# Performance work log

Hardware: AMD Instinct MI355X
Metric: run time of the kernel (lower is better)

Reference implementation:

```python
import jax, jax.numpy as jnp
import numpy as np

# Standard icosahedron face list (20 faces over 12 vertices).
ICO_FACES = np.array([
    [0, 11, 5], [0, 5, 1], [0, 1, 7], [0, 7, 10], [0, 10, 11],
    [1, 5, 9], [5, 11, 4], [11, 10, 2], [10, 7, 6], [7, 1, 8],
    [3, 9, 4], [3, 4, 2], [3, 2, 6], [3, 6, 8], [3, 8, 9],
    [4, 9, 5], [2, 4, 11], [6, 2, 10], [8, 6, 7], [9, 8, 1],
], dtype=np.int64)


def _ico_face_adjacency():
    # Faces are adjacent iff they share an edge == share exactly 2 vertices.
    adj = np.zeros((20, 20), dtype=np.float32)
    for i in range(20):
        for j in range(i + 1, 20):
            if len(set(ICO_FACES[i]) & set(ICO_FACES[j])) == 2:
                adj[i, j] = adj[j, i] = 1.0
    return jnp.asarray(adj)


def setup_inputs() -> dict:
    key = jax.random.key(0)
    ks = jax.random.split(key, 9)
    B, D = 65536, 512
    def w(k, fan_in, fan_out):
        return jax.random.normal(k, (fan_in, fan_out), jnp.float32) * (1.0 / np.sqrt(fan_in))
    return {
        "z": jax.random.normal(ks[0], (B, D), jnp.float32),
        "W1": w(ks[1], D, 512), "b1": jnp.zeros((512,), jnp.float32),
        "W2": w(ks[2], 512, 256), "b2": jnp.zeros((256,), jnp.float32),
        "W3": w(ks[3], 256, 128), "b3": jnp.zeros((128,), jnp.float32),
        "W4": w(ks[4], 128, 20), "b4": jnp.zeros((20,), jnp.float32),
        "precomputed_adj": _ico_face_adjacency(),  # [20,20], zero diagonal
    }


def reference(z, W1, b1, W2, b2, W3, b3, W4, b4, precomputed_adj):
    # Eval path: dropout = identity, recon_loss = 0.
    h = jax.nn.relu(z @ W1 + b1)
    h = jax.nn.relu(h @ W2 + b2)
    h = jax.nn.relu(h @ W3 + b3)
    face_probs = jax.nn.sigmoid(h @ W4 + b4)          # [B, 20]
    face_mask = (face_probs > 0.5).astype(z.dtype)    # [B, 20]
    # outer(mask, mask) * precomputed adjacency; diagonal of adj is already 0,
    # reproducing the i != j condition of the original triple loop.
    adj_matrix = face_mask[:, :, None] * face_mask[:, None, :] * precomputed_adj  # [B,20,20]
    recon_loss = jnp.asarray(0.0, jnp.float32)
    return (adj_matrix, face_mask, face_probs, recon_loss)
```

## Files before the change

kernel.cpp:

```cpp
#include <hip/hip_runtime.h>
#include <math.h>

#define NT   1024
#define BR   32
#define TAU  1e-3f
#define LIST_CAP 65536

typedef _Float16 half8 __attribute__((ext_vector_type(8)));
typedef float    f32x4 __attribute__((ext_vector_type(4)));

#define SWZ(r) (((r)&7)<<4)

#define PACK_ELS 425984
#define OFF_LIST 16
#define OFF_PH   (16 + LIST_CAP*4)
#define OFF_PL   (OFF_PH + PACK_ELS*2)
#define WS_PACK_NEED (OFF_PL + PACK_ELS*2)
#define WS_F32_NEED  (16 + LIST_CAP*4)

__device__ __forceinline__ int p1(int c){ return ((c&7)<<6)|(c>>3); }
__device__ __forceinline__ int p2(int c){ return ((c&3)<<6)|(c>>2); }
__device__ __forceinline__ int p3(int c){ return ((c&1)<<6)|(c>>1); }

__global__ void pack_w(const float* __restrict__ W1, const float* __restrict__ W2,
                       const float* __restrict__ W3,
                       _Float16* __restrict__ PH, _Float16* __restrict__ PL) {
    int i = blockIdx.x * 256 + threadIdx.x;
    if (i >= PACK_ELS) return;
    const float* W; int N, KS, loc;
    if (i < 262144)            { W = W1; N = 512; KS = 16; loc = i; }
    else if (i < 393216)       { W = W2; N = 256; KS = 16; loc = i - 262144; }
    else                       { W = W3; N = 128; KS = 8;  loc = i - 393216; }
    int j   = loc & 7;
    int l   = (loc >> 3) & 63;
    int rest = loc >> 9;
    int ks  = rest & (KS - 1);
    int nt  = rest >> (KS == 16 ? 4 : 3);
    int k = ks * 32 + (l >> 4) * 8 + j;
    int n = nt * 16 + (l & 15);
    float v = W[k * N + n];
    _Float16 hi = (_Float16)v;
    _Float16 lo = (_Float16)(v - (float)hi);
    PH[i] = hi; PL[i] = lo;
}

template<int K, int N, int NTW, int MREP, bool SPLIT_OUT>
__device__ __forceinline__ void mfma_layer(const char* __restrict__ actIn,
    const _Float16* __restrict__ PH, const _Float16* __restrict__ PL,
    const float* __restrict__ bias,
    char* __restrict__ actOut, float* __restrict__ h3out,
    int nt0, int m0, int l)
{
    constexpr int KS = K / 32;
    const int r  = l & 15;
    const int kg = l >> 4;
    f32x4 acc[MREP][NTW];
#pragma unroll
    for (int t = 0; t < NTW; ++t) {
        float bb = bias[(nt0 + t) * 16 + r];
#pragma unroll
        for (int m = 0; m < MREP; ++m) acc[m][t] = (f32x4){bb, bb, bb, bb};
    }
    constexpr int loIn = BR * K * 2;

#define AADDR(m, ks) ((((((m0 + (m)) * 16 + r) * K + kg * 8 + (ks) * 32) * 2) ^ SWZ((m0 + (m)) * 16 + r)))
#define BIDX(t, ks)  (((size_t)((nt0 + (t)) * KS + (ks)) * 64 + l) * 8)

    half8 ah0[MREP], al0[MREP];
    half8 bh0[NTW],  bl0[NTW];
    half8 bh1[NTW],  bl1[NTW];
#pragma unroll
    for (int m = 0; m < MREP; ++m) {
        int ao = AADDR(m, 0);
        ah0[m] = *(const half8*)(actIn + ao);
        al0[m] = *(const half8*)(actIn + ao + loIn);
    }
#pragma unroll
    for (int t = 0; t < NTW; ++t) {
        bh0[t] = *(const half8*)(PH + BIDX(t, 0));
        bl0[t] = *(const half8*)(PL + BIDX(t, 0));
        bh1[t] = *(const half8*)(PH + BIDX(t, 1));
        bl1[t] = *(const half8*)(PL + BIDX(t, 1));
    }

#pragma unroll
    for (int ks = 0; ks < KS; ++ks) {
        half8 bh2[NTW], bl2[NTW], ahn[MREP], aln[MREP];
        if (ks + 2 < KS) {
#pragma unroll
            for (int t = 0; t < NTW; ++t) {
                bh2[t] = *(const half8*)(PH + BIDX(t, ks + 2));
                bl2[t] = *(const half8*)(PL + BIDX(t, ks + 2));
            }
        }
        if (ks + 1 < KS) {
#pragma unroll
            for (int m = 0; m < MREP; ++m) {
                int ao = AADDR(m, ks + 1);
                ahn[m] = *(const half8*)(actIn + ao);
                aln[m] = *(const half8*)(actIn + ao + loIn);
            }
        }
#pragma unroll
        for (int t = 0; t < NTW; ++t)
#pragma unroll
            for (int m = 0; m < MREP; ++m) {
                acc[m][t] = __builtin_amdgcn_mfma_f32_16x16x32_f16(ah0[m], bh0[t], acc[m][t], 0, 0, 0);
                acc[m][t] = __builtin_amdgcn_mfma_f32_16x16x32_f16(ah0[m], bl0[t], acc[m][t], 0, 0, 0);
                acc[m][t] = __builtin_amdgcn_mfma_f32_16x16x32_f16(al0[m], bh0[t], acc[m][t], 0, 0, 0);
            }
#pragma unroll
        for (int t = 0; t < NTW; ++t) {
            bh0[t] = bh1[t]; bl0[t] = bl1[t];
            bh1[t] = bh2[t]; bl1[t] = bl2[t];
        }
#pragma unroll
        for (int m = 0; m < MREP; ++m) { ah0[m] = ahn[m]; al0[m] = aln[m]; }
    }
#undef AADDR
#undef BIDX

    constexpr int loOut = BR * N * 2;
#pragma unroll
    for (int t = 0; t < NTW; ++t) {
        int n = (nt0 + t) * 16 + r;
#pragma unroll
        for (int m = 0; m < MREP; ++m)
#pragma unroll
        for (int b = 0; b < 4; ++b) {
            int rowD = (m0 + m) * 16 + kg * 4 + b;
            float v = acc[m][t][b];
            v = v > 0.f ? v : 0.f;
            if constexpr (SPLIT_OUT) {
                _Float16 hi = (_Float16)v;
                _Float16 lo = (_Float16)(v - (float)hi);
                int lin = (rowD * N + n) * 2;
                int sw  = lin ^ SWZ(rowD);
                *(_Float16*)(actOut + sw)         = hi;
                *(_Float16*)(actOut + sw + loOut) = lo;
            } else {
                h3out[rowD * 132 + n] = v;
            }
        }
    }
}

__global__ __launch_bounds__(NT, 4)
void dec_mfma(const float* __restrict__ z,
              const float* __restrict__ b1, const float* __restrict__ b2,
              const float* __restrict__ b3,
              const float* __restrict__ W4, const float* __restrict__ b4,
              const float* __restrict__ adj,
              const _Float16* __restrict__ PH, const _Float16* __restrict__ PL,
              float* __restrict__ out, int B,
              int* __restrict__ cnt, int* __restrict__ list)
{
    __shared__ __align__(16) char ldsA[65536];
    __shared__ __align__(16) char ldsB[65536];
    __shared__ float logitsS[BR * 20];
    __shared__ float maskS[BR * 20];
    __shared__ float adjS[400];

    const int tid = threadIdx.x;
    const int w   = tid >> 6;
    const int l   = tid & 63;
    const int rowBase = blockIdx.x * BR;

    const int O_MASK  = B * 400;
    const int O_PROBS = O_MASK + B * 20;
    const int O_LOSS  = O_PROBS + B * 20;

    if (tid < 400) adjS[tid] = adj[tid];

    {
        int r   = tid >> 5;
        int c16 = (tid & 31) * 16;
        const float4* zp = (const float4*)(z + (size_t)(rowBase + r) * 512 + c16);
        float4 f0 = zp[0], f1 = zp[1], f2 = zp[2], f3 = zp[3];
        float fv[16] = {f0.x,f0.y,f0.z,f0.w, f1.x,f1.y,f1.z,f1.w,
                        f2.x,f2.y,f2.z,f2.w, f3.x,f3.y,f3.z,f3.w};
        half8 hi0, hi1, lo0, lo1;
#pragma unroll
        for (int j = 0; j < 8; ++j) {
            _Float16 h = (_Float16)fv[j];
            hi0[j] = h; lo0[j] = (_Float16)(fv[j] - (float)h);
        }
#pragma unroll
        for (int j = 0; j < 8; ++j) {
            _Float16 h = (_Float16)fv[8 + j];
            hi1[j] = h; lo1[j] = (_Float16)(fv[8 + j] - (float)h);
        }
        int lin = (r * 512 + c16) * 2;
        int swz = SWZ(r);
        *(half8*)(ldsA + ((lin     ) ^ swz))          = hi0;
        *(half8*)(ldsA + ((lin + 16) ^ swz))          = hi1;
        *(half8*)(ldsA + ((lin     ) ^ swz) + 32768)  = lo0;
        *(half8*)(ldsA + ((lin + 16) ^ swz) + 32768)  = lo1;
    }
    __syncthreads();

    mfma_layer<512, 512, 2, 2, true >(ldsA, PH,          PL,          b1, ldsB, nullptr, w * 2, 0, l);
    __syncthreads();
    mfma_layer<512, 256, 1, 2, true >(ldsB, PH + 262144, PL + 262144, b2, ldsA, nullptr, w, 0, l);
    __syncthreads();
    mfma_layer<256, 128, 1, 1, false>(ldsA, PH + 393216, PL + 393216, b3, nullptr, (float*)ldsB, w & 7, w >> 3, l);
    __syncthreads();

    const float* h3 = (const float*)ldsB;
    for (int o = tid; o < BR * 20; o += NT) {
        int r = o / 20, c = o - r * 20;
        float acc = b4[c];
        for (int k = 0; k < 128; ++k)
            acc += h3[r * 132 + k] * W4[k * 20 + c];
        logitsS[o] = acc;
    }
    __syncthreads();

    if (tid < BR) {
        float mn = 1e30f;
#pragma unroll
        for (int c = 0; c < 20; ++c)
            mn = fminf(mn, fabsf(logitsS[tid * 20 + c]));
        if (mn < TAU) {
            int idx = atomicAdd(cnt, 1);
            if (idx < LIST_CAP) list[idx] = rowBase + tid;
        }
    }

    for (int o = tid; o < BR * 20; o += NT) {
        double lg = (double)logitsS[o];
        double p  = 1.0 / (1.0 + exp(-lg));
        out[O_PROBS + rowBase * 20 + o] = (float)p;
        float m = lg > 0.0 ? 1.0f : 0.0f;
        out[O_MASK + rowBase * 20 + o] = m;
        maskS[o] = m;
    }
    __syncthreads();

    for (int o = tid; o < BR * 20; o += NT) {
        int r = o / 20, ii = o - r * 20;
        float mri = maskS[r * 20 + ii];
        float* orow = &out[(rowBase + r) * 400 + ii * 20];
#pragma unroll
        for (int b = 0; b < 5; ++b) {
            float4 v;
            v.x = mri * maskS[r * 20 + 4*b+0] * adjS[ii * 20 + 4*b+0];
            v.y = mri * maskS[r * 20 + 4*b+1] * adjS[ii * 20 + 4*b+1];
            v.z = mri * maskS[r * 20 + 4*b+2] * adjS[ii * 20 + 4*b+2];
            v.w = mri * maskS[r * 20 + 4*b+3] * adjS[ii * 20 + 4*b+3];
            *(float4*)&orow[4*b] = v;
        }
    }

    if (blockIdx.x == 0 && tid == 0) out[O_LOSS] = 0.0f;
}

template<typename T, bool FLAG>
__global__ __launch_bounds__(256, 2)
void dec_fused(const float* __restrict__ z,
               const float* __restrict__ W1, const float* __restrict__ b1,
               const float* __restrict__ W2, const float* __restrict__ b2,
               const float* __restrict__ W3, const float* __restrict__ b3,
               const float* __restrict__ W4, const float* __restrict__ b4,
               const float* __restrict__ adj,
               float* __restrict__ out, int B,
               int* __restrict__ cnt, int* __restrict__ list)
{
    constexpr int STR = (sizeof(T) == 4) ? 20 : 17;
    __shared__ T     hT[512 * STR];
    __shared__ T     logitsS[16 * 20];
    __shared__ float maskS[16 * 20];
    __shared__ float adjS[400];

    const int tid = threadIdx.x;
    const int rg  = tid >> 6;
    const int cg  = tid & 63;
    const int r0  = rg * 4;
    const int rowBase = blockIdx.x * 16;

    const int O_MASK  = B * 400;
    const int O_PROBS = O_MASK + B * 20;
    const int O_LOSS  = O_PROBS + B * 20;

    for (int i = tid; i < 400; i += 256) adjS[i] = adj[i];
    for (int i = tid; i < 512 * 16; i += 256) {
        int k = i & 511, r = i >> 9;
        hT[k * STR + r] = (T)z[(rowBase + r) * 512 + k];
    }
    __syncthreads();
    {
        T a[4][8];
#pragma unroll
        for (int ri = 0; ri < 4; ++ri)
#pragma unroll
            for (int ci = 0; ci < 8; ++ci) a[ri][ci] = (T)0;
#pragma unroll 2
        for (int k = 0; k < 512; ++k) {
            T zr[4];
#pragma unroll
            for (int ri = 0; ri < 4; ++ri) zr[ri] = hT[k * STR + r0 + ri];
            const float4* w1p = (const float4*)(W1 + k * 512 + cg * 8);
            float4 w0 = w1p[0], w1v = w1p[1];
            T wv[8] = {(T)w0.x,(T)w0.y,(T)w0.z,(T)w0.w,
                       (T)w1v.x,(T)w1v.y,(T)w1v.z,(T)w1v.w};
#pragma unroll
            for (int ci = 0; ci < 8; ++ci)
#pragma unroll
                for (int ri = 0; ri < 4; ++ri)
                    a[ri][ci] += zr[ri] * wv[ci];
        }
        __syncthreads();
#pragma unroll
        for (int ci = 0; ci < 8; ++ci) {
            int c = cg * 8 + ci;
            T bb = (T)b1[c]; int cp = p1(c);
#pragma unroll
            for (int ri = 0; ri < 4; ++ri) {
                T v = a[ri][ci] + bb;
                hT[cp * STR + r0 + ri] = v > (T)0 ? v : (T)0;
            }
        }
        __syncthreads();
    }
    {
        T a[4][4];
#pragma unroll
        for (int ri = 0; ri < 4; ++ri)
#pragma unroll
            for (int ci = 0; ci < 4; ++ci) a[ri][ci] = (T)0;
#pragma unroll 2
        for (int k = 0; k < 512; ++k) {
            int kp = p1(k);
            T zr[4];
#pragma unroll
            for (int ri = 0; ri < 4; ++ri) zr[ri] = hT[kp * STR + r0 + ri];
            float4 wq = *(const float4*)(W2 + k * 256 + cg * 4);
            T wv[4] = {(T)wq.x,(T)wq.y,(T)wq.z,(T)wq.w};
#pragma unroll
            for (int ci = 0; ci < 4; ++ci)
#pragma unroll
                for (int ri = 0; ri < 4; ++ri)
                    a[ri][ci] += zr[ri] * wv[ci];
        }
        __syncthreads();
#pragma unroll
        for (int ci = 0; ci < 4; ++ci) {
            int c = cg * 4 + ci;
            T bb = (T)b2[c]; int cp = p2(c);
#pragma unroll
            for (int ri = 0; ri < 4; ++ri) {
                T v = a[ri][ci] + bb;
                hT[cp * STR + r0 + ri] = v > (T)0 ? v : (T)0;
            }
        }
        __syncthreads();
    }
    {
        T a[4][2];
#pragma unroll
        for (int ri = 0; ri < 4; ++ri)
#pragma unroll
            for (int ci = 0; ci < 2; ++ci) a[ri][ci] = (T)0;
#pragma unroll 2
        for (int k = 0; k < 256; ++k) {
            int kp = p2(k);
            T zr[4];
#pragma unroll
            for (int ri = 0; ri < 4; ++ri) zr[ri] = hT[kp * STR + r0 + ri];
            float2 wq = *(const float2*)(W3 + k * 128 + cg * 2);
            T wv[2] = {(T)wq.x,(T)wq.y};
#pragma unroll
            for (int ci = 0; ci < 2; ++ci)
#pragma unroll
                for (int ri = 0; ri < 4; ++ri)
                    a[ri][ci] += zr[ri] * wv[ci];
        }
        __syncthreads();
#pragma unroll
        for (int ci = 0; ci < 2; ++ci) {
            int c = cg * 2 + ci;
            T bb = (T)b3[c]; int cp = p3(c);
#pragma unroll
            for (int ri = 0; ri < 4; ++ri) {
                T v = a[ri][ci] + bb;
                hT[cp * STR + r0 + ri] = v > (T)0 ? v : (T)0;
            }
        }
        __syncthreads();
    }
    for (int o = tid; o < 16 * 20; o += 256) {
        int r = o / 20, c = o - r * 20;
        T acc = (T)b4[c];
        for (int k = 0; k < 128; ++k)
            acc += hT[p3(k) * STR + r] * (T)W4[k * 20 + c];
        logitsS[o] = acc;
    }
    __syncthreads();
    if constexpr (FLAG) {
        if (tid < 16) {
            float mn = 1e30f;
#pragma unroll
            for (int c = 0; c < 20; ++c)
                mn = fminf(mn, fabsf((float)logitsS[tid * 20 + c]));
            if (mn < TAU) {
                int idx = atomicAdd(cnt, 1);
                if (idx < LIST_CAP) list[idx] = rowBase + tid;
            }
        }
    }
    for (int o = tid; o < 16 * 20; o += 256) {
        double lg = (double)logitsS[o];
        double p  = 1.0 / (1.0 + exp(-lg));
        out[O_PROBS + rowBase * 20 + o] = (float)p;
        float m = lg > 0.0 ? 1.0f : 0.0f;
        out[O_MASK + rowBase * 20 + o] = m;
        maskS[o] = m;
    }
    __syncthreads();
    for (int o = tid; o < 16 * 20; o += 256) {
        int r = o / 20, ii = o - r * 20;
        float mri = maskS[r * 20 + ii];
        float* orow = &out[(rowBase + r) * 400 + ii * 20];
#pragma unroll
        for (int b = 0; b < 5; ++b) {
            float4 v;
            v.x = mri * maskS[r * 20 + 4*b+0] * adjS[ii * 20 + 4*b+0];
            v.y = mri * maskS[r * 20 + 4*b+1] * adjS[ii * 20 + 4*b+1];
            v.z = mri * maskS[r * 20 + 4*b+2] * adjS[ii * 20 + 4*b+2];
            v.w = mri * maskS[r * 20 + 4*b+3] * adjS[ii * 20 + 4*b+3];
            *(float4*)&orow[4*b] = v;
        }
    }
    if (blockIdx.x == 0 && tid == 0) out[O_LOSS] = 0.0f;
}

__global__ __launch_bounds__(256, 4)
void repair_rows(const float* __restrict__ z,
                 const float* __restrict__ W1, const float* __restrict__ b1,
                 const float* __restrict__ W2, const float* __restrict__ b2,
                 const float* __restrict__ W3, const float* __restrict__ b3,
                 const float* __restrict__ W4, const float* __restrict__ b4,
                 const float* __restrict__ adj,
                 float* __restrict__ out, int B,
                 const int* __restrict__ cnt, const int* __restrict__ list)
{
    __shared__ double bufA[512];
    __shared__ double bufB[512];
    __shared__ double lgS[20];
    __shared__ float  mskS[20];

    const int tid = threadIdx.x;
    const int O_MASK  = B * 400;
    const int O_PROBS = O_MASK + B * 20;

    int n = *cnt;
    if (n > LIST_CAP) n = LIST_CAP;

    for (int i = blockIdx.x; i < n; i += gridDim.x) {
        int row = list[i];
        for (int k = tid; k < 512; k += 256)
            bufA[k] = (double)z[(size_t)row * 512 + k];
        __syncthreads();
        {
            int c0 = tid, c1 = tid + 256;
            double a0 = (double)b1[c0], a1 = (double)b1[c1];
            for (int k = 0; k < 512; ++k) {
                double h = bufA[k];
                a0 += h * (double)W1[k * 512 + c0];
                a1 += h * (double)W1[k * 512 + c1];
            }
            __syncthreads();
            bufB[c0] = a0 > 0.0 ? a0 : 0.0;
            bufB[c1] = a1 > 0.0 ? a1 : 0.0;
            __syncthreads();
        }
        {
            double a0 = (double)b2[tid < 256 ? tid : 0];
            if (tid < 256)
                for (int k = 0; k < 512; ++k)
                    a0 += bufB[k] * (double)W2[k * 256 + tid];
            __syncthreads();
            if (tid < 256) bufA[tid] = a0 > 0.0 ? a0 : 0.0;
            __syncthreads();
        }
        {
            double a0 = (double)b3[tid < 128 ? tid : 0];
            if (tid < 128)
                for (int k = 0; k < 256; ++k)
                    a0 += bufA[k] * (double)W3[k * 128 + tid];
            __syncthreads();
            if (tid < 128) bufB[tid] = a0 > 0.0 ? a0 : 0.0;
            __syncthreads();
        }
        if (tid < 20) {
            double a0 = (double)b4[tid];
            for (int k = 0; k < 128; ++k)
                a0 += bufB[k] * (double)W4[k * 20 + tid];
            lgS[tid] = a0;
        }
        __syncthreads();
        if (tid < 20) {
            double lg = lgS[tid];
            out[O_PROBS + (size_t)row * 20 + tid] = (float)(1.0 / (1.0 + exp(-lg)));
            float m = lg > 0.0 ? 1.0f : 0.0f;
            out[O_MASK + (size_t)row * 20 + tid] = m;
            mskS[tid] = m;
        }
        __syncthreads();
        for (int o = tid; o < 400; o += 256) {
            int ii = o / 20, jj = o - ii * 20;
            out[(size_t)row * 400 + o] = mskS[ii] * mskS[jj] * adj[o];
        }
        __syncthreads();
    }
}

extern "C" void kernel_launch(void* const* d_in, const int* in_sizes, int n_in,
                              void* d_out, int out_size, void* d_ws, size_t ws_size,
                              hipStream_t stream) {
    const float* z   = (const float*)d_in[0];
    const float* W1  = (const float*)d_in[1];
    const float* b1  = (const float*)d_in[2];
    const float* W2  = (const float*)d_in[3];
    const float* b2  = (const float*)d_in[4];
    const float* W3  = (const float*)d_in[5];
    const float* b3  = (const float*)d_in[6];
    const float* W4  = (const float*)d_in[7];
    const float* b4  = (const float*)d_in[8];
    const float* adj = (const float*)d_in[9];
    float* out = (float*)d_out;

    const int B = in_sizes[0] / 512;

    if (ws_size >= (size_t)WS_PACK_NEED) {
        int* cnt  = (int*)d_ws;
        int* list = (int*)((char*)d_ws + OFF_LIST);
        _Float16* PH = (_Float16*)((char*)d_ws + OFF_PH);
        _Float16* PL = (_Float16*)((char*)d_ws + OFF_PL);
        hipMemsetAsync(d_ws, 0, 16, stream);
        hipLaunchKernelGGL(pack_w, dim3((PACK_ELS + 255) / 256), dim3(256), 0, stream,
                           W1, W2, W3, PH, PL);
        hipLaunchKernelGGL(dec_mfma, dim3(B / BR), dim3(NT), 0, stream,
                           z, b1, b2, b3, W4, b4, adj, PH, PL, out, B, cnt, list);
        hipLaunchKernelGGL(repair_rows, dim3(1024), dim3(256), 0, stream,
                           z, W1, b1, W2, b2, W3, b3, W4, b4, adj, out, B, cnt, list);
    } else if (ws_size >= (size_t)WS_F32_NEED) {
        int* cnt  = (int*)d_ws;
        int* list = (int*)((char*)d_ws + OFF_LIST);
        hipMemsetAsync(d_ws, 0, 16, stream);
        hipLaunchKernelGGL((dec_fused<float, true>), dim3(B / 16), dim3(256), 0, stream,
                           z, W1, b1, W2, b2, W3, b3, W4, b4, adj, out, B, cnt, list);
        hipLaunchKernelGGL(repair_rows, dim3(1024), dim3(256), 0, stream,
                           z, W1, b1, W2, b2, W3, b3, W4, b4, adj, out, B, cnt, list);
    } else {
        hipLaunchKernelGGL((dec_fused<double, false>), dim3(B / 16), dim3(256), 0, stream,
                           z, W1, b1, W2, b2, W3, b3, W4, b4, adj, out, B,
                           (int*)nullptr, (int*)nullptr);
    }
}
```

Baseline: 455.6 us.

## Hand-schedule weight prefetch with inline asm loads and explicit vmcnt waits

Replaces the compiler-scheduled weight-fragment prefetch with inline-asm global_load_dwordx4 into a three-slot ring buffer. Explicit s_waitcnt vmcnt counts and sched_barriers keep two k-steps of weight loads in flight across the MFMA block. Activation LDS reads move to the current k-step instead of being prefetched one step ahead, and s_setprio raises wave priority around the MFMA burst. This aims to stop the compiler from serializing or conservatively waiting on loads, at the cost of fragile hand-tuned wait counts and more exposed LDS latency.

After: 446.8 us. No clear change (-1.9%).

```diff
diff --git a/kernel.cpp b/kernel.cpp
--- a/kernel.cpp
+++ b/kernel.cpp
@@ -8,6 +8,7 @@
 
 typedef _Float16 half8 __attribute__((ext_vector_type(8)));
 typedef float    f32x4 __attribute__((ext_vector_type(4)));
+typedef unsigned int u32x4 __attribute__((ext_vector_type(4)));
 
 #define SWZ(r) (((r)&7)<<4)
 
@@ -44,6 +45,19 @@
     PH[i] = hi; PL[i] = lo;
 }
 
+__device__ __forceinline__ u32x4 agl(const _Float16* p) {
+    u32x4 d;
+    asm volatile("global_load_dwordx4 %0, %1, off" : "=v"(d) : "v"(p));
+    return d;
+}
+template<int NWAIT> __device__ __forceinline__ void waitv() {
+    if constexpr (NWAIT == 0)      asm volatile("s_waitcnt vmcnt(0)");
+    else if constexpr (NWAIT == 2) asm volatile("s_waitcnt vmcnt(2)");
+    else if constexpr (NWAIT == 4) asm volatile("s_waitcnt vmcnt(4)");
+    else                           asm volatile("s_waitcnt vmcnt(8)");
+    __builtin_amdgcn_sched_barrier(0);
+}
+
 template<int K, int N, int NTW, int MREP, bool SPLIT_OUT>
 __device__ __forceinline__ void mfma_layer(const char* __restrict__ actIn,
     const _Float16* __restrict__ PH, const _Float16* __restrict__ PL,
@@ -51,7 +65,8 @@
     char* __restrict__ actOut, float* __restrict__ h3out,
     int nt0, int m0, int l)
 {
-    constexpr int KS = K / 32;
+    constexpr int KS    = K / 32;
+    constexpr int BATCH = 2 * NTW;
     const int r  = l & 15;
     const int kg = l >> 4;
     f32x4 acc[MREP][NTW];
@@ -61,64 +76,56 @@
 #pragma unroll
         for (int m = 0; m < MREP; ++m) acc[m][t] = (f32x4){bb, bb, bb, bb};
     }
+    __builtin_amdgcn_sched_barrier(0);
     constexpr int loIn = BR * K * 2;
 
 #define AADDR(m, ks) ((((((m0 + (m)) * 16 + r) * K + kg * 8 + (ks) * 32) * 2) ^ SWZ((m0 + (m)) * 16 + r)))
-#define BIDX(t, ks)  (((size_t)((nt0 + (t)) * KS + (ks)) * 64 + l) * 8)
-
-    half8 ah0[MREP], al0[MREP];
-    half8 bh0[NTW],  bl0[NTW];
-    half8 bh1[NTW],  bl1[NTW];
-#pragma unroll
-    for (int m = 0; m < MREP; ++m) {
-        int ao = AADDR(m, 0);
-        ah0[m] = *(const half8*)(actIn + ao);
-        al0[m] = *(const half8*)(actIn + ao + loIn);
-    }
-#pragma unroll
-    for (int t = 0; t < NTW; ++t) {
-        bh0[t] = *(const half8*)(PH + BIDX(t, 0));
-        bl0[t] = *(const half8*)(PL + BIDX(t, 0));
-        bh1[t] = *(const half8*)(PH + BIDX(t, 1));
-        bl1[t] = *(const half8*)(PL + BIDX(t, 1));
-    }
+#define BOFF(t, ks)  (((size_t)((nt0 + (t)) * KS + (ks)) * 64 + l) * 8)
+
+    u32x4 Bh[3][NTW], Bl[3][NTW];
+#pragma unroll
+    for (int t = 0; t < NTW; ++t) { Bh[0][t] = agl(PH + BOFF(t, 0)); Bl[0][t] = agl(PL + BOFF(t, 0)); }
+#pragma unroll
+    for (int t = 0; t < NTW; ++t) { Bh[1][t] = agl(PH + BOFF(t, 1)); Bl[1][t] = agl(PL + BOFF(t, 1)); }
 
 #pragma unroll
     for (int ks = 0; ks < KS; ++ks) {
-        half8 bh2[NTW], bl2[NTW], ahn[MREP], aln[MREP];
+        const int cur = ks % 3, nx = (ks + 2) % 3;
         if (ks + 2 < KS) {
 #pragma unroll
             for (int t = 0; t < NTW; ++t) {
-                bh2[t] = *(const half8*)(PH + BIDX(t, ks + 2));
-                bl2[t] = *(const half8*)(PL + BIDX(t, ks + 2));
-            }
-        }
-        if (ks + 1 < KS) {
+                Bh[nx][t] = agl(PH + BOFF(t, ks + 2));
+                Bl[nx][t] = agl(PL + BOFF(t, ks + 2));
+            }
+        }
+        half8 ah[MREP], al[MREP];
+#pragma unroll
+        for (int m = 0; m < MREP; ++m) {
+            int ao = AADDR(m, ks);
+            ah[m] = *(const half8*)(actIn + ao);
+            al[m] = *(const half8*)(actIn + ao + loIn);
+        }
+        const int rem = KS - 1 - ks;
+        if (rem >= 2)      waitv<2 * BATCH>();
+        else if (rem == 1) waitv<BATCH>();
+        else               waitv<0>();
+        __builtin_amdgcn_s_setprio(1);
+#pragma unroll
+        for (int t = 0; t < NTW; ++t) {
+            half8 bh = __builtin_bit_cast(half8, Bh[cur][t]);
+            half8 bl = __builtin_bit_cast(half8, Bl[cur][t]);
 #pragma unroll
             for (int m = 0; m < MREP; ++m) {
-                int ao = AADDR(m, ks + 1);
-                ahn[m] = *(const half8*)(actIn + ao);
-                aln[m] = *(const half8*)(actIn + ao + loIn);
-            }
-        }
-#pragma unroll
-        for (int t = 0; t < NTW; ++t)
-#pragma unroll
-            for (int m = 0; m < MREP; ++m) {
-                acc[m][t] = __builtin_amdgcn_mfma_f32_16x16x32_f16(ah0[m], bh0[t], acc[m][t], 0, 0, 0);
-                acc[m][t] = __builtin_amdgcn_mfma_f32_16x16x32_f16(ah0[m], bl0[t], acc[m][t], 0, 0, 0);
-                acc[m][t] = __builtin_amdgcn_mfma_f32_16x16x32_f16(al0[m], bh0[t], acc[m][t], 0, 0, 0);
-            }
-#pragma unroll
-        for (int t = 0; t < NTW; ++t) {
-            bh0[t] = bh1[t]; bl0[t] = bl1[t];
-            bh1[t] = bh2[t]; bl1[t] = bl2[t];
-        }
-#pragma unroll
-        for (int m = 0; m < MREP; ++m) { ah0[m] = ahn[m]; al0[m] = aln[m]; }
+                acc[m][t] = __builtin_amdgcn_mfma_f32_16x16x32_f16(ah[m], bh, acc[m][t], 0, 0, 0);
+                acc[m][t] = __builtin_amdgcn_mfma_f32_16x16x32_f16(ah[m], bl, acc[m][t], 0, 0, 0);
+                acc[m][t] = __builtin_amdgcn_mfma_f32_16x16x32_f16(al[m], bh, acc[m][t], 0, 0, 0);
+            }
+        }
+        __builtin_amdgcn_s_setprio(0);
+        __builtin_amdgcn_sched_barrier(0);
     }
 #undef AADDR
-#undef BIDX
+#undef BOFF
 
     constexpr int loOut = BR * N * 2;
 #pragma unroll
```
